# Kernel tuning notes

Hardware: AMD Instinct MI355X
Metric: run time of the kernel (lower is better)

Reference implementation:

```python
import jax, jax.numpy as jnp
import numpy as np

TEMPERATURE = 0.5
EPS = 1e-8  # matches torch cosine_similarity eps guard semantics (norm clamp)


def setup_inputs() -> dict:
    key = jax.random.key(0)
    k1, k2 = jax.random.split(key)
    B, D = 4096, 256
    z_i = jax.random.normal(k1, (B, D), dtype=jnp.float32)
    z_j = jax.random.normal(k2, (B, D), dtype=jnp.float32)
    return {"z_i": z_i, "z_j": z_j}


def reference(z_i, z_j):
    B = z_i.shape[0]
    z = jnp.concatenate([z_i, z_j], axis=0)            # [2B, D]
    # cosine similarity: normalize once, then GEMM
    norm = jnp.maximum(jnp.linalg.norm(z, axis=1, keepdims=True), EPS)
    zn = z / norm                                       # [2B, D]
    sim = zn @ zn.T                                     # [2B, 2B]
    # positives: diag(sim, +B) and diag(sim, -B)
    idx = jnp.arange(B)
    sim_ij = sim[idx, idx + B]
    sim_ji = sim[idx + B, idx]
    positives = jnp.concatenate([sim_ij, sim_ji])       # [2B]
    # masked denominator: exclude self-similarity
    mask = 1.0 - jnp.eye(2 * B, dtype=sim.dtype)
    denom = jnp.sum(mask * jnp.exp(sim / TEMPERATURE), axis=1)  # [2B]
    all_losses = -jnp.log(jnp.exp(positives / TEMPERATURE) / denom)
    return jnp.sum(all_losses) / (2 * B)
```

## Files before the change

kernel.cpp:

```cpp
#include <hip/hip_runtime.h>
#include <hip/hip_bf16.h>
#include <cstdint>
#include <cstddef>
#include <math.h>

#define D 256
#define TEMP_INV 2.0f
#define EPS_NORM 1e-8f
#define NTILES 2080

typedef __attribute__((ext_vector_type(8))) short bf16x8;
typedef __attribute__((ext_vector_type(4))) float f32x4;

__global__ void __launch_bounds__(256) normalize_rows(
    const float* __restrict__ zi, const float* __restrict__ zj,
    __hip_bfloat16* __restrict__ zn, float* __restrict__ denom, int B) {
  const int wid = threadIdx.x >> 6;
  const int lane = threadIdx.x & 63;
  if (threadIdx.x < 16) denom[blockIdx.x * 16 + threadIdx.x] = 0.0f;
#pragma unroll
  for (int it = 0; it < 4; ++it) {
    int row = it * 2048 + blockIdx.x * 4 + wid;
    const float* src = (row < B) ? (zi + (size_t)row * D)
                                 : (zj + (size_t)(row - B) * D);
    float4 v = ((const float4*)src)[lane];
    float ss = v.x * v.x + v.y * v.y + v.z * v.z + v.w * v.w;
    for (int off = 32; off; off >>= 1) ss += __shfl_xor(ss, off);
    float rn = 1.0f / fmaxf(sqrtf(ss), EPS_NORM);
    union { ushort4 u; __hip_bfloat16 h[4]; } o;
    o.h[0] = __float2bfloat16(v.x * rn);
    o.h[1] = __float2bfloat16(v.y * rn);
    o.h[2] = __float2bfloat16(v.z * rn);
    o.h[3] = __float2bfloat16(v.w * rn);
    ((ushort4*)zn)[(size_t)row * (D / 4) + lane] = o.u;
  }
}

__device__ __forceinline__ void decode_tile(int t, int Nb, int& by, int& bx) {
  float fb = (2.0f * Nb + 1.0f -
              sqrtf((float)((2 * Nb + 1) * (2 * Nb + 1) - 8 * t))) * 0.5f;
  int y = (int)fb;
  while ((y + 1) * Nb - ((y + 1) * y) / 2 <= t) ++y;
  while (y * Nb - (y * (y - 1)) / 2 > t) --y;
  by = y;
  bx = y + (t - (y * Nb - (y * (y - 1)) / 2));
}

__global__ void __launch_bounds__(256, 3) ntxent_gemm(
    const __hip_bfloat16* __restrict__ zn,
    float* __restrict__ denom, float* __restrict__ pos, int B) {
  __shared__ __align__(16) __hip_bfloat16 Ash[128 * 64];
  __shared__ __align__(16) __hip_bfloat16 Bsh[128 * 64];

  const int Nb = (2 * B) / 128;
  int by, bx;
  decode_tile(blockIdx.x, Nb, by, bx);
  const int bm = by * 128;
  const int bn = bx * 128;
  const bool isDiag = (by == bx);
  const bool isPos = (bx == by + B / 128);

  const int tid = threadIdx.x;
  const int wid = tid >> 6;
  const int lane = tid & 63;
  const int wy = wid >> 1, wx = wid & 1;
  const int wrow0 = wid * 32;

  const int lr = lane >> 3;
  const int c8 = lane & 7;

  const int frow = lane & 15;
  const int quad = lane >> 4;
  const int f7 = frow & 7;

  f32x4 acc[4][4] = {};

  const __hip_bfloat16* gA = zn + (size_t)(bm + wrow0 + lr) * D + c8 * 8;
  const __hip_bfloat16* gB = zn + (size_t)(bn + wrow0 + lr) * D + c8 * 8;
  const int ldsoff = (wrow0 + lr) * 64 + (c8 ^ lr) * 8;

  float4 va0 = *(const float4*)(gA + 0 * 8 * D);
  float4 va1 = *(const float4*)(gA + 1 * 8 * D);
  float4 va2 = *(const float4*)(gA + 2 * 8 * D);
  float4 va3 = *(const float4*)(gA + 3 * 8 * D);
  float4 vb0 = *(const float4*)(gB + 0 * 8 * D);
  float4 vb1 = *(const float4*)(gB + 1 * 8 * D);
  float4 vb2 = *(const float4*)(gB + 2 * 8 * D);
  float4 vb3 = *(const float4*)(gB + 3 * 8 * D);

#pragma unroll
  for (int k0i = 0; k0i < 4; ++k0i) {
    __syncthreads();
    *(float4*)&Ash[ldsoff + 0 * 8 * 64] = va0;
    *(float4*)&Ash[ldsoff + 1 * 8 * 64] = va1;
    *(float4*)&Ash[ldsoff + 2 * 8 * 64] = va2;
    *(float4*)&Ash[ldsoff + 3 * 8 * 64] = va3;
    *(float4*)&Bsh[ldsoff + 0 * 8 * 64] = vb0;
    *(float4*)&Bsh[ldsoff + 1 * 8 * 64] = vb1;
    *(float4*)&Bsh[ldsoff + 2 * 8 * 64] = vb2;
    *(float4*)&Bsh[ldsoff + 3 * 8 * 64] = vb3;
    __syncthreads();
    if (k0i < 3) {
      const int k0 = (k0i + 1) * 64;
      va0 = *(const float4*)(gA + 0 * 8 * D + k0);
      va1 = *(const float4*)(gA + 1 * 8 * D + k0);
      va2 = *(const float4*)(gA + 2 * 8 * D + k0);
      va3 = *(const float4*)(gA + 3 * 8 * D + k0);
      vb0 = *(const float4*)(gB + 0 * 8 * D + k0);
      vb1 = *(const float4*)(gB + 1 * 8 * D + k0);
      vb2 = *(const float4*)(gB + 2 * 8 * D + k0);
      vb3 = *(const float4*)(gB + 3 * 8 * D + k0);
    }
#pragma unroll
    for (int kk = 0; kk < 2; ++kk) {
      bf16x8 a[4], b[4];
#pragma unroll
      for (int i = 0; i < 4; ++i)
        a[i] = *(const bf16x8*)
            &Ash[(wy * 64 + i * 16 + frow) * 64 + ((kk * 4 + quad) ^ f7) * 8];
#pragma unroll
      for (int j = 0; j < 4; ++j)
        b[j] = *(const bf16x8*)
            &Bsh[(wx * 64 + j * 16 + frow) * 64 + ((kk * 4 + quad) ^ f7) * 8];
#pragma unroll
      for (int i = 0; i < 4; ++i)
#pragma unroll
        for (int j = 0; j < 4; ++j)
          acc[i][j] =
              __builtin_amdgcn_mfma_f32_16x16x32_bf16(a[i], b[j], acc[i][j], 0, 0, 0);
    }
  }

  const int colq = lane & 15;
  float cs[4] = {0.0f, 0.0f, 0.0f, 0.0f};
#pragma unroll
  for (int i = 0; i < 4; ++i) {
#pragma unroll
    for (int r = 0; r < 4; ++r) {
      int row = bm + wy * 64 + i * 16 + quad * 4 + r;
      float rs = 0.0f;
#pragma unroll
      for (int j = 0; j < 4; ++j) {
        int col = bn + wx * 64 + j * 16 + colq;
        float v = acc[i][j][r];
        float e = __expf(v * TEMP_INV);
        e = (isDiag && col == row) ? 0.0f : e;
        rs += e;
        cs[j] += e;
        if (isPos && col == row + B) { pos[row] = v; pos[col] = v; }
      }
      rs += __shfl_xor(rs, 1);
      rs += __shfl_xor(rs, 2);
      rs += __shfl_xor(rs, 4);
      rs += __shfl_xor(rs, 8);
      if (colq == 0) atomicAdd(&denom[row], rs);
    }
  }
  if (!isDiag) {
#pragma unroll
    for (int j = 0; j < 4; ++j) {
      float c = cs[j];
      c += __shfl_xor(c, 16);
      c += __shfl_xor(c, 32);
      if (quad == 0) atomicAdd(&denom[bn + wx * 64 + j * 16 + colq], c);
    }
  }
}

__global__ void __launch_bounds__(1024) finalize(
    const float* __restrict__ denom, const float* __restrict__ pos,
    float* __restrict__ out, int N) {
  __shared__ float red[16];
  const int tid = threadIdx.x;
  float s = 0.0f;
  for (int i = tid; i < N / 4; i += 1024) {
    float4 d = ((const float4*)denom)[i];
    float4 p = ((const float4*)pos)[i];
    s += __logf(d.x) - p.x * TEMP_INV;
    s += __logf(d.y) - p.y * TEMP_INV;
    s += __logf(d.z) - p.z * TEMP_INV;
    s += __logf(d.w) - p.w * TEMP_INV;
  }
  for (int off = 32; off; off >>= 1) s += __shfl_xor(s, off);
  if ((tid & 63) == 0) red[tid >> 6] = s;
  __syncthreads();
  if (tid < 16) {
    s = red[tid];
    s += __shfl_xor(s, 1);
    s += __shfl_xor(s, 2);
    s += __shfl_xor(s, 4);
    s += __shfl_xor(s, 8);
    if (tid == 0) out[0] = s / (float)N;
  }
}

extern "C" void kernel_launch(void* const* d_in, const int* in_sizes, int n_in,
                              void* d_out, int out_size, void* d_ws, size_t ws_size,
                              hipStream_t stream) {
  const float* zi = (const float*)d_in[0];
  const float* zj = (const float*)d_in[1];
  const int B = in_sizes[0] / D;
  const int N = 2 * B;

  __hip_bfloat16* zn = (__hip_bfloat16*)d_ws;
  float* denom = (float*)((char*)d_ws + (size_t)N * D * sizeof(__hip_bfloat16));
  float* pos = denom + N;

  normalize_rows<<<512, 256, 0, stream>>>(zi, zj, zn, denom, B);
  ntxent_gemm<<<NTILES, 256, 0, stream>>>(zn, denom, pos, B);
  finalize<<<1, 1024, 0, stream>>>(denom, pos, (float*)d_out, N);
}
```

Before: 108.2 us.

## Replace global atomic denominators with per-tile partial sums and parallel finalize

The GEMM epilogue no longer issues global atomicAdds per row and column. Row and column exp-sums are reduced through shared memory and written to a partial-sum buffer indexed by tile block. The finalize kernel now runs across many blocks, each summing 64 partials per row, taking the log, and atomically adding into the output. Occupancy hint raised to 4 blocks per SM. This trades atomic contention for an extra 2MB partial buffer read/write and one more block sync.

```diff
diff --git a/kernel.cpp b/kernel.cpp
--- a/kernel.cpp
+++ b/kernel.cpp
@@ -14,10 +14,10 @@
 
 __global__ void __launch_bounds__(256) normalize_rows(
     const float* __restrict__ zi, const float* __restrict__ zj,
-    __hip_bfloat16* __restrict__ zn, float* __restrict__ denom, int B) {
+    __hip_bfloat16* __restrict__ zn, float* __restrict__ out, int B) {
   const int wid = threadIdx.x >> 6;
   const int lane = threadIdx.x & 63;
-  if (threadIdx.x < 16) denom[blockIdx.x * 16 + threadIdx.x] = 0.0f;
+  if (blockIdx.x == 0 && threadIdx.x == 0) out[0] = 0.0f;
 #pragma unroll
   for (int it = 0; it < 4; ++it) {
     int row = it * 2048 + blockIdx.x * 4 + wid;
@@ -46,13 +46,14 @@
   bx = y + (t - (y * Nb - (y * (y - 1)) / 2));
 }
 
-__global__ void __launch_bounds__(256, 3) ntxent_gemm(
+__global__ void __launch_bounds__(256, 4) ntxent_gemm(
     const __hip_bfloat16* __restrict__ zn,
-    float* __restrict__ denom, float* __restrict__ pos, int B) {
+    float* __restrict__ part, float* __restrict__ pos, int B) {
   __shared__ __align__(16) __hip_bfloat16 Ash[128 * 64];
   __shared__ __align__(16) __hip_bfloat16 Bsh[128 * 64];
 
-  const int Nb = (2 * B) / 128;
+  const int N = 2 * B;
+  const int Nb = N / 128;
   int by, bx;
   decode_tile(blockIdx.x, Nb, by, bx);
   const int bm = by * 128;
@@ -131,13 +132,17 @@
     }
   }
 
+  __syncthreads();
+  float* red = (float*)Ash;
+
   const int colq = lane & 15;
   float cs[4] = {0.0f, 0.0f, 0.0f, 0.0f};
 #pragma unroll
   for (int i = 0; i < 4; ++i) {
 #pragma unroll
     for (int r = 0; r < 4; ++r) {
-      int row = bm + wy * 64 + i * 16 + quad * 4 + r;
+      int rowloc = wy * 64 + i * 16 + quad * 4 + r;
+      int row = bm + rowloc;
       float rs = 0.0f;
 #pragma unroll
       for (int j = 0; j < 4; ++j) {
@@ -153,44 +158,41 @@
       rs += __shfl_xor(rs, 2);
       rs += __shfl_xor(rs, 4);
       rs += __shfl_xor(rs, 8);
-      if (colq == 0) atomicAdd(&denom[row], rs);
+      if (colq == 0) red[rowloc * 2 + wx] = rs;
     }
   }
-  if (!isDiag) {
-#pragma unroll
-    for (int j = 0; j < 4; ++j) {
-      float c = cs[j];
-      c += __shfl_xor(c, 16);
-      c += __shfl_xor(c, 32);
-      if (quad == 0) atomicAdd(&denom[bn + wx * 64 + j * 16 + colq], c);
-    }
-  }
-}
-
-__global__ void __launch_bounds__(1024) finalize(
-    const float* __restrict__ denom, const float* __restrict__ pos,
+#pragma unroll
+  for (int j = 0; j < 4; ++j) {
+    float c = cs[j];
+    c += __shfl_xor(c, 16);
+    c += __shfl_xor(c, 32);
+    if (quad == 0) red[256 + (wx * 64 + j * 16 + colq) * 2 + wy] = c;
+  }
+  __syncthreads();
+  if (tid < 128) {
+    part[(size_t)bx * N + bm + tid] = red[tid * 2] + red[tid * 2 + 1];
+  } else if (!isDiag) {
+    int t = tid - 128;
+    part[(size_t)by * N + bn + t] = red[256 + t * 2] + red[256 + t * 2 + 1];
+  }
+}
+
+__global__ void __launch_bounds__(256) finalize(
+    const float* __restrict__ part, const float* __restrict__ pos,
     float* __restrict__ out, int N) {
-  __shared__ float red[16];
-  const int tid = threadIdx.x;
+  const int idx = blockIdx.x * 256 + threadIdx.x;
+  const int NS = N / 128;
   float s = 0.0f;
-  for (int i = tid; i < N / 4; i += 1024) {
-    float4 d = ((const float4*)denom)[i];
-    float4 p = ((const float4*)pos)[i];
-    s += __logf(d.x) - p.x * TEMP_INV;
-    s += __logf(d.y) - p.y * TEMP_INV;
-    s += __logf(d.z) - p.z * TEMP_INV;
-    s += __logf(d.w) - p.w * TEMP_INV;
-  }
-  for (int off = 32; off; off >>= 1) s += __shfl_xor(s, off);
-  if ((tid & 63) == 0) red[tid >> 6] = s;
+#pragma unroll 8
+  for (int k = 0; k < NS; ++k) s += part[(size_t)k * N + idx];
+  float loss = __logf(s) - pos[idx] * TEMP_INV;
+  for (int off = 32; off; off >>= 1) loss += __shfl_xor(loss, off);
+  __shared__ float redsh[4];
+  if ((threadIdx.x & 63) == 0) redsh[threadIdx.x >> 6] = loss;
   __syncthreads();
-  if (tid < 16) {
-    s = red[tid];
-    s += __shfl_xor(s, 1);
-    s += __shfl_xor(s, 2);
-    s += __shfl_xor(s, 4);
-    s += __shfl_xor(s, 8);
-    if (tid == 0) out[0] = s / (float)N;
+  if (threadIdx.x == 0) {
+    float t = redsh[0] + redsh[1] + redsh[2] + redsh[3];
+    atomicAdd(out, t / (float)N);
   }
 }
 
@@ -203,10 +205,10 @@
   const int N = 2 * B;
 
   __hip_bfloat16* zn = (__hip_bfloat16*)d_ws;
-  float* denom = (float*)((char*)d_ws + (size_t)N * D * sizeof(__hip_bfloat16));
-  float* pos = denom + N;
-
-  normalize_rows<<<512, 256, 0, stream>>>(zi, zj, zn, denom, B);
-  ntxent_gemm<<<NTILES, 256, 0, stream>>>(zn, denom, pos, B);
-  finalize<<<1, 1024, 0, stream>>>(denom, pos, (float*)d_out, N);
-}
+  float* pos = (float*)((char*)d_ws + (size_t)N * D * sizeof(__hip_bfloat16));
+  float* part = pos + N;
+
+  normalize_rows<<<512, 256, 0, stream>>>(zi, zj, zn, (float*)d_out, B);
+  ntxent_gemm<<<NTILES, 256, 0, stream>>>(zn, part, pos, B);
+  finalize<<<N / 256, 256, 0, stream>>>(part, pos, (float*)d_out, N);
+}
```

Result: faster. 99.00 us (-8.5%).
